# Optimization experiments

Hardware: AMD Instinct MI355X
Metric: run time of the kernel (lower is better)

Reference implementation:

```python
import jax, jax.numpy as jnp
import numpy as np

K_NEIGHBORS = 30
MAX_FLOAT = float(np.finfo(np.float32).max)
DIST_EPS = 1e-6


def setup_inputs() -> dict:
    key = jax.random.key(0)
    k1, k2 = jax.random.split(key)
    # X: (B, N, n_grid_square_types, 3) coordinates; scaled to spread points out
    X = jax.random.normal(k1, (1, 8192, 4, 3), dtype=jnp.float32) * 10.0
    # C: chain/field map; C > 0 means valid node (field_map_to_mask)
    C = jax.random.randint(k2, (1, 8192), 0, 4)
    return {"X": X, "C": C}


def _pairwise_dist(Xc):
    # Xc: (B, N, 3) centroid coordinates -> (B, N, N) Euclidean distances
    sq = jnp.sum(Xc * Xc, axis=-1)                      # (B, N)
    G = jnp.einsum('bnd,bmd->bnm', Xc, Xc)              # Gram matrix (GEMM)
    D2 = sq[:, :, None] + sq[:, None, :] - 2.0 * G
    return jnp.sqrt(jnp.maximum(D2, 0.0) + DIST_EPS)


def reference(X, C):
    # distance_grid_square_type < 0 -> centroid over grid-square types
    Xc = jnp.mean(X, axis=2)                            # (B, N, 3)
    D = _pairwise_dist(Xc)                              # (B, N, N)

    # node mask and 2D edge mask (mask_full = mask_i * mask_j)
    mask_1d = (C > 0).astype(jnp.float32)               # (B, N)
    mask_2d = mask_1d[:, :, None] * mask_1d[:, None, :]  # (B, N, N)

    # masked distances: invalid edges pushed to +max_float
    D_masked = mask_2d * D + (1.0 - mask_2d) * MAX_FLOAT

    # topk smallest distances via top_k on negated values
    neg_vals, edge_idx = jax.lax.top_k(-D_masked, K_NEIGHBORS)
    edge_D = -neg_vals                                  # (B, N, K)

    # graph.collect_edges: gather edge mask at neighbor indices
    mask_ij = jnp.take_along_axis(mask_2d, edge_idx, axis=-1)  # (B, N, K)

    return edge_idx, edge_D, mask_ij
```

## Files before the change

### kernel.cpp

```cpp
#include <hip/hip_runtime.h>
#include <hip/hip_bf16.h>
#include <stdint.h>

typedef unsigned long long u64;
typedef float f32x2 __attribute__((ext_vector_type(2)));
typedef float f32x4 __attribute__((ext_vector_type(4)));

#define N 8192
#define K 30
#define NWAVE 4
#define NSLOT 9
#define CAP 576
#define FLUSH_AT 320


static __device__ __forceinline__ f32x2 pk_mul(f32x2 a, f32x2 b) {
  f32x2 d; asm("v_pk_mul_f32 %0, %1, %2" : "=v"(d) : "v"(a), "v"(b)); return d;
}
static __device__ __forceinline__ f32x2 pk_add(f32x2 a, f32x2 b) {
  f32x2 d; asm("v_pk_add_f32 %0, %1, %2" : "=v"(d) : "v"(a), "v"(b)); return d;
}
static __device__ __forceinline__ f32x2 pk_fma(f32x2 a, f32x2 b, f32x2 c) {
  f32x2 d; asm("v_pk_fma_f32 %0, %1, %2, %3" : "=v"(d) : "v"(a), "v"(b), "v"(c)); return d;
}
static __device__ __forceinline__ f32x2 clamp0(f32x2 a) {
  f32x2 d; d.x = fmaxf(a.x, 0.0f); d.y = fmaxf(a.y, 0.0f); return d;
}

__global__ void zero_kernel(int* __restrict__ ctr) {
  if (threadIdx.x < 2) ctr[threadIdx.x] = 0;
}

__global__ __launch_bounds__(256) void prep_kernel(const float* __restrict__ X,
                                                   const int* __restrict__ C,
                                                   float* __restrict__ gx,
                                                   float* __restrict__ gy,
                                                   float* __restrict__ gz,
                                                   float* __restrict__ gw,
                                                   int* __restrict__ gid,
                                                   int* __restrict__ ctr) {
  int i = blockIdx.x * 256 + threadIdx.x;
  if (i >= N) return;
  const float4* xp = (const float4*)(X + (size_t)i * 12);
  float4 f0 = xp[0], f1 = xp[1], f2 = xp[2];
  float mx = __fmul_rn(__fadd_rn(__fadd_rn(__fadd_rn(f0.x, f0.w), f1.z), f2.y), 0.25f);
  float my = __fmul_rn(__fadd_rn(__fadd_rn(__fadd_rn(f0.y, f1.x), f1.w), f2.z), 0.25f);
  float mz = __fmul_rn(__fadd_rn(__fadd_rn(__fadd_rn(f0.z, f1.y), f2.x), f2.w), 0.25f);
  float sq = __fadd_rn(__fadd_rn(__fmul_rn(mx, mx), __fmul_rn(my, my)), __fmul_rn(mz, mz));
  bool valid = (C[i] > 0);
  int p;
  if (valid) p = atomicAdd(&ctr[0], 1);
  else       p = N - 1 - atomicAdd(&ctr[1], 1);
  gx[p] = mx; gy[p] = my; gz[p] = mz;
  gw[p] = valid ? sq : __builtin_inff();
  gid[p] = i;
}

static __device__ __forceinline__ u64 sort64(u64 v, int lane) {
#pragma unroll
  for (int kk = 2; kk <= 64; kk <<= 1) {
#pragma unroll
    for (int j = kk >> 1; j > 0; j >>= 1) {
      u64 o = __shfl_xor(v, j);
      bool lower = (lane & j) == 0;
      bool asc = (lane & kk) == 0;
      u64 mn = v < o ? v : o;
      u64 mx = v < o ? o : v;
      v = (lower == asc) ? mn : mx;
    }
  }
  return v;
}
static __device__ __forceinline__ u64 merge64(u64 L, u64 v, int lane) {
  u64 vr = __shfl(v, 63 - lane);
  u64 m = L < vr ? L : vr;
#pragma unroll
  for (int j = 32; j > 0; j >>= 1) {
    u64 o = __shfl_xor(m, j);
    bool lower = (lane & j) == 0;
    u64 mn = m < o ? m : o;
    u64 mx = m < o ? o : m;
    m = lower ? mn : mx;
  }
  return m;
}

static __device__ __forceinline__ unsigned mbcnt64(u64 mask) {
  return __builtin_amdgcn_mbcnt_hi((unsigned)(mask >> 32),
         __builtin_amdgcn_mbcnt_lo((unsigned)mask, 0u));
}

__device__ __forceinline__ void radix_flush(float& th, unsigned& cnt,
                                            unsigned* bd, unsigned* bj, int lane) {
  unsigned h[NSLOT], j[NSLOT];
#pragma unroll
  for (int s = 0; s < NSLOT; ++s) {
    bool in = (unsigned)(lane + 64 * s) < cnt;
    h[s] = in ? bd[lane + 64 * s] : 0xFFFFFFFFu;
    j[s] = in ? bj[lane + 64 * s] : 0u;
  }
  unsigned piv = 0;
#pragma unroll
  for (int b = 15; b >= 0; --b) {
    unsigned cand = piv + (0x10000u << b);
    int c = 0;
#pragma unroll
    for (int s = 0; s < NSLOT; ++s) c += __popcll(__ballot(h[s] < cand));
    if (c < K) piv = cand;
  }
  if (piv < 0xFFFF0000u)
    th = fminf(th, __uint_as_float(piv + 0x10000u));

  const unsigned thb = __float_as_uint(th);
  unsigned total = 0;
#pragma unroll
  for (int s = 0; s < NSLOT; ++s) {
    u64 mk = __ballot(h[s] < thb);
    if (mk) {
      unsigned pos = total + mbcnt64(mk);
      if (h[s] < thb) { bd[pos] = h[s]; bj[pos] = j[s]; }
      total += (unsigned)__popcll(mk);
    }
  }
  cnt = total;
}

__device__ __forceinline__ u64 finalize_row(float& th, unsigned& cnt,
                                            unsigned* bd, unsigned* bj,
                                            const int* __restrict__ gid, int lane) {
  radix_flush(th, cnt, bd, bj, lane);
  u64 L = ~0ull;
  for (unsigned base = 0; base < cnt; base += 64) {
    u64 v = ~0ull;
    if (base + (unsigned)lane < cnt) {
      float d2c = __uint_as_float(bd[base + lane]);
      float D = sqrtf(__fadd_rn(d2c, 1e-6f));
      unsigned jo = (unsigned)gid[bj[base + lane]];
      v = ((u64)__float_as_uint(D) << 32) | jo;
    }
    v = sort64(v, lane);
    L = merge64(L, v, lane);
  }
  return L;
}

#define PROC_NB(MASK, PRED, DV, JJ)                                           \
  { unsigned pos = cnt + mbcnt64(MASK);                                       \
    if (PRED) { bd[pos] = __float_as_uint(DV); bj[pos] = (JJ); }              \
    cnt += (unsigned)__popcll(MASK); }

__device__ __forceinline__ void write_row(int r, bool act, u64 L, int lane,
                                          __hip_bfloat16* __restrict__ out) {
  if (lane >= K) return;
  const int o = r * K + lane;
  if (act) {
    out[o] = __float2bfloat16((float)(unsigned)(L & 0xFFFFFFFFull));
    out[N * K + o] = __float2bfloat16(__uint_as_float((unsigned)(L >> 32)));
    out[2 * N * K + o] = __float2bfloat16(1.0f);
  } else {
    out[o] = __float2bfloat16((float)lane);
    ((unsigned short*)out)[N * K + o] = 0x7F7Fu;
    out[2 * N * K + o] = __float2bfloat16(0.0f);
  }
}

__global__ __launch_bounds__(256) void knn_kernel(const float* __restrict__ gx,
                                                  const float* __restrict__ gy,
                                                  const float* __restrict__ gz,
                                                  const float* __restrict__ gw,
                                                  const int* __restrict__ gid,
                                                  const int* __restrict__ ctr,
                                                  __hip_bfloat16* __restrict__ out) {
  __shared__ unsigned bufD[NWAVE][CAP];
  __shared__ unsigned bufJ[NWAVE][CAP];

  const int lane = threadIdx.x & 63;
  const int w = threadIdx.x >> 6;
  const int nValid = ctr[0];
  const int pos = blockIdx.x * NWAVE + w;
  const int rout = gid[pos];
  const bool act = pos < nValid;

  if (!act) {
    write_row(rout, false, 0, lane, out);
    return;
  }

  const float qx = gx[pos], qy = gy[pos], qz = gz[pos], qw = gw[pos];
  const f32x2 qx2 = {qx, qx}, qy2 = {qy, qy}, qz2 = {qz, qz}, qw2 = {qw, qw};
  const f32x2 neg1 = {-1.0f, -1.0f};

  float th = __builtin_inff();
  unsigned cnt = 0;
  unsigned* bd = &bufD[w][0];
  unsigned* bj = &bufJ[w][0];

  const f32x4* bx4 = (const f32x4*)gx;
  const f32x4* by4 = (const f32x4*)gy;
  const f32x4* bz4 = (const f32x4*)gz;
  const f32x4* bw4 = (const f32x4*)gw;

  const int niter = (nValid + 255) >> 8;

  f32x4 AX, AY, AZ, AW, BX, BY, BZ, BW;
#define LOADS(P, B4)                                                           \
  P##X = bx4[(B4) + lane]; P##Y = by4[(B4) + lane];                            \
  P##Z = bz4[(B4) + lane]; P##W = bw4[(B4) + lane];

  LOADS(A, 0)
  LOADS(B, 64)

#define ITERX(P, IT, PRIME)                                                    \
  {                                                                            \
    const int bb4 = (IT) * 64;                                                 \
    f32x2 xlo = {P##X.x, P##X.y}, xhi = {P##X.z, P##X.w};                      \
    f32x2 ylo = {P##Y.x, P##Y.y}, yhi = {P##Y.z, P##Y.w};                      \
    f32x2 zlo = {P##Z.x, P##Z.y}, zhi = {P##Z.z, P##Z.w};                      \
    f32x2 wlo = {P##W.x, P##W.y}, whi = {P##W.z, P##W.w};                      \
    f32x2 dtl = pk_add(pk_add(pk_mul(qx2, xlo), pk_mul(qy2, ylo)),             \
                       pk_mul(qz2, zlo));                                      \
    f32x2 dlo = clamp0(pk_fma(pk_add(dtl, dtl), neg1, pk_add(qw2, wlo)));      \
    f32x2 dth = pk_add(pk_add(pk_mul(qx2, xhi), pk_mul(qy2, yhi)),             \
                       pk_mul(qz2, zhi));                                      \
    f32x2 dhi = clamp0(pk_fma(pk_add(dth, dth), neg1, pk_add(qw2, whi)));      \
    LOADS(P, bb4 + 128)    \
    float mn = fminf(fminf(dlo.x, dlo.y), fminf(dhi.x, dhi.y));                \
    if (PRIME && nValid >= 256) {                                              \
      float l = mn;                                                            \
      _Pragma("unroll")                                                        \
      for (int d = 32; d; d >>= 1) l = fmaxf(l, __shfl_xor(l, d));             \
      th = l;          \
    }                                                                          \
    u64 anym = __ballot(mn <= th);                                             \
    if (anym) {                                                                \
      bool p0 = dlo.x <= th, p1 = dlo.y <= th, p2 = dhi.x <= th, p3 = dhi.y <= th; \
      u64 m0 = __ballot(p0), m1 = __ballot(p1);                                \
      u64 m2 = __ballot(p2), m3 = __ballot(p3);                                \
      const unsigned j0 = (unsigned)(4 * (bb4 + lane));                        \
      PROC_NB(m0, p0, dlo.x, j0)                                               \
      PROC_NB(m1, p1, dlo.y, j0 + 1)                                           \
      PROC_NB(m2, p2, dhi.x, j0 + 2)                                           \
      PROC_NB(m3, p3, dhi.y, j0 + 3)                                           \
      if (cnt > FLUSH_AT) radix_flush(th, cnt, bd, bj, lane);                  \
    }                                                                          \
  }

  ITERX(A, 0, true)
  if (niter > 1) ITERX(B, 1, false)
  int it = 2;
#pragma unroll 1
  for (; it + 1 < niter; it += 2) {
    ITERX(A, it, false)
    ITERX(B, it + 1, false)
  }
  if (it < niter) ITERX(A, it, false)

  u64 L = finalize_row(th, cnt, bd, bj, gid, lane);
  write_row(rout, true, L, lane, out);
}

extern "C" void kernel_launch(void* const* d_in, const int* in_sizes, int n_in,
                              void* d_out, int out_size, void* d_ws, size_t ws_size,
                              hipStream_t stream) {
  const float* X = (const float*)d_in[0];
  const int* C = (const int*)d_in[1];
  float* gx = (float*)d_ws;
  float* gy = (float*)((char*)d_ws + 32768);
  float* gz = (float*)((char*)d_ws + 65536);
  float* gw = (float*)((char*)d_ws + 98304);
  int* gid = (int*)((char*)d_ws + 131072);
  int* ctr = (int*)((char*)d_ws + 163840);
  __hip_bfloat16* out = (__hip_bfloat16*)d_out;

  zero_kernel<<<1, 64, 0, stream>>>(ctr);
  prep_kernel<<<N / 256, 256, 0, stream>>>(X, C, gx, gy, gz, gw, gid, ctr);
  knn_kernel<<<N / NWAVE, 256, 0, stream>>>(gx, gy, gz, gw, gid, ctr, out);
}
```

Baseline: 56.11 us.

## Process 512 candidates per iteration and shrink blocks to two waves

Each iteration now covers two 256-point groups per lane, with double-buffered loads for both, so the threshold check and ballot gate are amortized over more candidates and more loads are in flight. Blocks drop to two waves with a larger per-wave shared buffer and a lower flush threshold. More points per pass raises register pressure. Candidates accepted under a stale threshold can pile up more between flushes, and the priming threshold is taken from a larger sample, which makes it looser.

```diff
diff --git a/kernel.cpp b/kernel.cpp
--- a/kernel.cpp
+++ b/kernel.cpp
@@ -8,10 +8,10 @@
 
 #define N 8192
 #define K 30
-#define NWAVE 4
-#define NSLOT 9
-#define CAP 576
-#define FLUSH_AT 320
+#define NWAVE 2
+#define NSLOT 11
+#define CAP 704
+#define FLUSH_AT 192
 
 
 static __device__ __forceinline__ f32x2 pk_mul(f32x2 a, f32x2 b) {
@@ -164,7 +164,7 @@
   }
 }
 
-__global__ __launch_bounds__(256) void knn_kernel(const float* __restrict__ gx,
+__global__ __launch_bounds__(128) void knn_kernel(const float* __restrict__ gx,
                                                   const float* __restrict__ gy,
                                                   const float* __restrict__ gz,
                                                   const float* __restrict__ gw,
@@ -200,32 +200,43 @@
   const f32x4* bz4 = (const f32x4*)gz;
   const f32x4* bw4 = (const f32x4*)gw;
 
-  const int niter = (nValid + 255) >> 8;
-
-  f32x4 AX, AY, AZ, AW, BX, BY, BZ, BW;
+  const int niter = (nValid + 511) >> 9;
+
+  f32x4 A0X, A0Y, A0Z, A0W, A1X, A1Y, A1Z, A1W;
+  f32x4 B0X, B0Y, B0Z, B0W, B1X, B1Y, B1Z, B1W;
 #define LOADS(P, B4)                                                           \
-  P##X = bx4[(B4) + lane]; P##Y = by4[(B4) + lane];                            \
-  P##Z = bz4[(B4) + lane]; P##W = bw4[(B4) + lane];
+  P##0X = bx4[(B4) + lane]; P##0Y = by4[(B4) + lane];                          \
+  P##0Z = bz4[(B4) + lane]; P##0W = bw4[(B4) + lane];                          \
+  P##1X = bx4[(B4) + 64 + lane]; P##1Y = by4[(B4) + 64 + lane];                \
+  P##1Z = bz4[(B4) + 64 + lane]; P##1W = bw4[(B4) + 64 + lane];
 
   LOADS(A, 0)
-  LOADS(B, 64)
+  LOADS(B, 128)
+
+#define D2G(GX, GY, GZ, GW, DLO, DHI)                                          \
+  {                                                                            \
+    f32x2 xlo = {GX.x, GX.y}, xhi = {GX.z, GX.w};                              \
+    f32x2 ylo = {GY.x, GY.y}, yhi = {GY.z, GY.w};                              \
+    f32x2 zlo = {GZ.x, GZ.y}, zhi = {GZ.z, GZ.w};                              \
+    f32x2 wlo = {GW.x, GW.y}, whi = {GW.z, GW.w};                              \
+    f32x2 dtl = pk_add(pk_add(pk_mul(qx2, xlo), pk_mul(qy2, ylo)),             \
+                       pk_mul(qz2, zlo));                                      \
+    DLO = clamp0(pk_fma(pk_add(dtl, dtl), neg1, pk_add(qw2, wlo)));            \
+    f32x2 dth = pk_add(pk_add(pk_mul(qx2, xhi), pk_mul(qy2, yhi)),             \
+                       pk_mul(qz2, zhi));                                      \
+    DHI = clamp0(pk_fma(pk_add(dth, dth), neg1, pk_add(qw2, whi)));            \
+  }
 
 #define ITERX(P, IT, PRIME)                                                    \
   {                                                                            \
-    const int bb4 = (IT) * 64;                                                 \
-    f32x2 xlo = {P##X.x, P##X.y}, xhi = {P##X.z, P##X.w};                      \
-    f32x2 ylo = {P##Y.x, P##Y.y}, yhi = {P##Y.z, P##Y.w};                      \
-    f32x2 zlo = {P##Z.x, P##Z.y}, zhi = {P##Z.z, P##Z.w};                      \
-    f32x2 wlo = {P##W.x, P##W.y}, whi = {P##W.z, P##W.w};                      \
-    f32x2 dtl = pk_add(pk_add(pk_mul(qx2, xlo), pk_mul(qy2, ylo)),             \
-                       pk_mul(qz2, zlo));                                      \
-    f32x2 dlo = clamp0(pk_fma(pk_add(dtl, dtl), neg1, pk_add(qw2, wlo)));      \
-    f32x2 dth = pk_add(pk_add(pk_mul(qx2, xhi), pk_mul(qy2, yhi)),             \
-                       pk_mul(qz2, zhi));                                      \
-    f32x2 dhi = clamp0(pk_fma(pk_add(dth, dth), neg1, pk_add(qw2, whi)));      \
-    LOADS(P, bb4 + 128)    \
-    float mn = fminf(fminf(dlo.x, dlo.y), fminf(dhi.x, dhi.y));                \
-    if (PRIME && nValid >= 256) {                                              \
+    const int bb4 = (IT) * 128;                                                \
+    f32x2 d0lo, d0hi, d1lo, d1hi;                                              \
+    D2G(P##0X, P##0Y, P##0Z, P##0W, d0lo, d0hi)                                \
+    D2G(P##1X, P##1Y, P##1Z, P##1W, d1lo, d1hi)                                \
+    LOADS(P, bb4 + 256)    \
+    float mn = fminf(fminf(fminf(d0lo.x, d0lo.y), fminf(d0hi.x, d0hi.y)),      \
+                     fminf(fminf(d1lo.x, d1lo.y), fminf(d1hi.x, d1hi.y)));     \
+    if (PRIME && nValid >= 512) {                                              \
       float l = mn;                                                            \
       _Pragma("unroll")                                                        \
       for (int d = 32; d; d >>= 1) l = fmaxf(l, __shfl_xor(l, d));             \
@@ -233,14 +244,24 @@
     }                                                                          \
     u64 anym = __ballot(mn <= th);                                             \
     if (anym) {                                                                \
-      bool p0 = dlo.x <= th, p1 = dlo.y <= th, p2 = dhi.x <= th, p3 = dhi.y <= th; \
+      bool p0 = d0lo.x <= th, p1 = d0lo.y <= th;                               \
+      bool p2 = d0hi.x <= th, p3 = d0hi.y <= th;                               \
+      bool p4 = d1lo.x <= th, p5 = d1lo.y <= th;                               \
+      bool p6 = d1hi.x <= th, p7 = d1hi.y <= th;                               \
       u64 m0 = __ballot(p0), m1 = __ballot(p1);                                \
       u64 m2 = __ballot(p2), m3 = __ballot(p3);                                \
+      u64 m4 = __ballot(p4), m5 = __ballot(p5);                                \
+      u64 m6 = __ballot(p6), m7 = __ballot(p7);                                \
       const unsigned j0 = (unsigned)(4 * (bb4 + lane));                        \
-      PROC_NB(m0, p0, dlo.x, j0)                                               \
-      PROC_NB(m1, p1, dlo.y, j0 + 1)                                           \
-      PROC_NB(m2, p2, dhi.x, j0 + 2)                                           \
-      PROC_NB(m3, p3, dhi.y, j0 + 3)                                           \
+      const unsigned j1 = j0 + 256;                                            \
+      PROC_NB(m0, p0, d0lo.x, j0)                                              \
+      PROC_NB(m1, p1, d0lo.y, j0 + 1)                                          \
+      PROC_NB(m2, p2, d0hi.x, j0 + 2)                                          \
+      PROC_NB(m3, p3, d0hi.y, j0 + 3)                                          \
+      PROC_NB(m4, p4, d1lo.x, j1)                                              \
+      PROC_NB(m5, p5, d1lo.y, j1 + 1)                                          \
+      PROC_NB(m6, p6, d1hi.x, j1 + 2)                                          \
+      PROC_NB(m7, p7, d1hi.y, j1 + 3)                                          \
       if (cnt > FLUSH_AT) radix_flush(th, cnt, bd, bj, lane);                  \
     }                                                                          \
   }
@@ -274,5 +295,5 @@
 
   zero_kernel<<<1, 64, 0, stream>>>(ctr);
   prep_kernel<<<N / 256, 256, 0, stream>>>(X, C, gx, gy, gz, gw, gid, ctr);
-  knn_kernel<<<N / NWAVE, 256, 0, stream>>>(gx, gy, gz, gw, gid, ctr, out);
-}
+  knn_kernel<<<N / NWAVE, 128, 0, stream>>>(gx, gy, gz, gw, gid, ctr, out);
+}
```

After: 67.18 us. 19.7% more time.
